# Kernel tuning notes

Measured on AMD Instinct MI355X. Metric: run time of the kernel, lower is better.

## Reference

```python
import jax, jax.numpy as jnp
import numpy as np

HEADS = 8

def setup_inputs() -> dict:
    key = jax.random.key(0)
    k1, k2, k3 = jax.random.split(key, 3)
    B, C, L = 8, 512, 4096
    dim_head = 64
    hidden = HEADS * dim_head  # 512
    x = jax.random.normal(k1, (B, C, L), dtype=jnp.float32)
    # Conv1d(dim, hidden*3, 1, bias=False) -> weight [hidden*3, dim]
    w_qkv = jax.random.normal(k2, (hidden * 3, C), dtype=jnp.float32) * 0.02
    # Conv1d(hidden, dim, 1) -> weight [dim, hidden], bias [dim]
    w_out = jax.random.normal(k3, (C, hidden), dtype=jnp.float32) * 0.02
    b_out = jnp.zeros((C,), dtype=jnp.float32)
    return {"x": x, "w_qkv": w_qkv, "w_out": w_out, "b_out": b_out}

def reference(x, w_qkv, w_out, b_out):
    B, C, L = x.shape
    # 1x1 Conv1d == channel matmul
    qkv = jnp.einsum('oc,bcl->bol', w_qkv, x)            # [B, 3*H*dh, L]
    qkv = qkv.reshape(B, 3, HEADS, -1, L)                # qkv outermost, then heads, then c
    q, k, v = qkv[:, 0], qkv[:, 1], qkv[:, 2]            # each [B, H, dh, L]
    k = jax.nn.softmax(k, axis=-1)                       # softmax over sequence
    context = jnp.einsum('bhdn,bhen->bhde', k, v)        # [B, H, dh, dh]
    out = jnp.einsum('bhde,bhdn->bhen', context, q)      # [B, H, dh, L]
    out = out.reshape(B, -1, L)                          # [B, H*dh, L]
    return jnp.einsum('oc,bcl->bol', w_out, out) + b_out[None, :, None]
```

## Files before the change

### kernel.cpp

```cpp
#include <hip/hip_runtime.h>
#include <hip/hip_bf16.h>


typedef __bf16 bf16x8 __attribute__((ext_vector_type(8)));
typedef __bf16 bf16x4 __attribute__((ext_vector_type(4)));
typedef float  f32x4  __attribute__((ext_vector_type(4)));

#define B_  8
#define L_  4096
#define C_  512

#define GLD_LDS16(g, l)                                             \
    __builtin_amdgcn_global_load_lds(                               \
        (const __attribute__((address_space(1))) void*)(g),         \
        (__attribute__((address_space(3))) void*)(l), 16, 0, 0)

#define FENCE asm volatile("" ::: "memory")
#define BAR   do { FENCE; __builtin_amdgcn_s_barrier(); FENCE; } while (0)
#define DRAIN_LGKM asm volatile("s_waitcnt lgkmcnt(0)" ::: "memory")
#define WAIT_VM(N) asm volatile("s_waitcnt vmcnt(" #N ")" ::: "memory")

__global__ __launch_bounds__(256) void prep_all(const float* __restrict__ x,
                                                __hip_bfloat16* __restrict__ xt,
                                                const float* __restrict__ wqkv_f,
                                                __hip_bfloat16* __restrict__ wkv_b,
                                                __hip_bfloat16* __restrict__ wqT) {
    __shared__ float tile[64 * 132];
    int blk = blockIdx.x;
    int t = threadIdx.x;
    if (blk < 2048) {
        int b = blk >> 8, rem = blk & 255;
        int l0 = (rem & 31) * 128, c0 = (rem >> 5) * 64;
        const float* xp = x + ((size_t)b * C_ + c0) * L_ + l0;
#pragma unroll
        for (int p = 0; p < 8; p++) {
            int i = p * 8 + (t >> 5);
            int j = (t & 31) * 4;
            float4 vv = *(const float4*)(xp + (size_t)i * L_ + j);
            *(float4*)&tile[i * 132 + j] = vv;
        }
        __syncthreads();
        unsigned short* xo = (unsigned short*)xt + ((size_t)b * L_ + l0) * C_ + c0;
#pragma unroll
        for (int qq = 0; qq < 8; qq++) {
            int l = qq * 16 + (t >> 4);
            int cg = (t & 15) * 4;
            bf16x4 ov;
#pragma unroll
            for (int k = 0; k < 4; k++) ov[k] = (__bf16)tile[(cg + k) * 132 + l];
            *(bf16x4*)(xo + (size_t)l * C_ + cg) = ov;
        }
    } else if (blk < 4096) {
        int i = (blk - 2048) * 256 + t;
        wkv_b[i] = __float2bfloat16(wqkv_f[512 * 512 + i]);
    } else {
        int tb = blk - 4096;
        int r0 = (tb >> 4) * 32, c0 = (tb & 15) * 32;
        int tx = t & 31, ty = t >> 5;
        for (int r = 0; r < 32; r += 8)
            tile[(ty + r) * 33 + tx] = wqkv_f[(size_t)(r0 + ty + r) * 512 + c0 + tx];
        __syncthreads();
        for (int r = 0; r < 32; r += 8)
            wqT[(size_t)(c0 + ty + r) * 512 + r0 + tx] = __float2bfloat16(tile[tx * 33 + ty + r]);
    }
}

template <int MODE>
__global__ __launch_bounds__(256, 2) void gemm_p(
    const __hip_bfloat16* __restrict__ A, const __hip_bfloat16* __restrict__ Bt,
    size_t strideA, size_t strideB, int M, int N, int K,
    __hip_bfloat16* __restrict__ kb, __hip_bfloat16* __restrict__ vb,
    float* __restrict__ outb, const float* __restrict__ bias) {
    __shared__ alignas(16) unsigned short sA[2][128 * 64];
    __shared__ alignas(16) unsigned short sB[2][128 * 64];

    int b = blockIdx.z;
    int m0 = blockIdx.y * 128, n0 = blockIdx.x * 128;
    const __hip_bfloat16* Ab = A + strideA * (size_t)b;
    const __hip_bfloat16* Bb = Bt + strideB * (size_t)b;

    int t = threadIdx.x;
    int lane = t & 63, wv = t >> 6;
    int l16 = lane & 15, q4 = lane >> 4;
    int wr = (wv >> 1) * 64, wc = (wv & 1) * 64;

    int srow = lane >> 3;
    int swz  = ((lane & 7) ^ srow) * 8;

    const __hip_bfloat16* gA[4];
    const __hip_bfloat16* gB[4];
    unsigned ldoff[4];
#pragma unroll
    for (int c = 0; c < 4; c++) {
        int r = c * 32 + wv * 8;
        gA[c] = Ab + (size_t)(m0 + r + srow) * K + swz;
        gB[c] = Bb + (size_t)(n0 + r + srow) * K + swz;
        ldoff[c] = (unsigned)r * 64;
    }

    int gsel0 = (q4 ^ (l16 & 7)) * 8;
    int gsel1 = gsel0 ^ 32;
    unsigned rA = (unsigned)(wr + l16) * 64;
    unsigned rB = (unsigned)(wc + l16) * 64;
    int NKT = K >> 6;

    f32x4 acc[4][4] = {};
    bf16x8 aF[4][2], bF[4][2];

#pragma unroll
    for (int c = 0; c < 4; c++) GLD_LDS16(gA[c], &sA[0][ldoff[c]]);
#pragma unroll
    for (int c = 0; c < 4; c++) GLD_LDS16(gB[c], &sB[0][ldoff[c]]);
    if (NKT > 1) {
#pragma unroll
        for (int c = 0; c < 4; c++) GLD_LDS16(gA[c] + 64, &sA[1][ldoff[c]]);
        WAIT_VM(4);
    } else {
        WAIT_VM(0);
    }
    BAR;

#pragma unroll 1
    for (int kt = 0; kt < NKT; ++kt) {
        int cur = kt & 1, nbuf = cur ^ 1;
        const unsigned short* As_b = sA[cur];
        const unsigned short* Bs_b = sB[cur];
        bool st1 = (kt + 1) < NKT;
        bool st2 = (kt + 2) < NKT;

#pragma unroll
        for (int i = 0; i < 4; i++) {
            aF[i][0] = *(const bf16x8*)&As_b[rA + i * 1024 + gsel0];
            aF[i][1] = *(const bf16x8*)&As_b[rA + i * 1024 + gsel1];
        }
#pragma unroll
        for (int j = 0; j < 2; j++) {
            bF[j][0] = *(const bf16x8*)&Bs_b[rB + j * 1024 + gsel0];
            bF[j][1] = *(const bf16x8*)&Bs_b[rB + j * 1024 + gsel1];
        }
        if (st1) {
            int ko = (kt + 1) << 6;
#pragma unroll
            for (int c = 0; c < 4; c++) GLD_LDS16(gB[c] + ko, &sB[nbuf][ldoff[c]]);
        }
        BAR;
        __builtin_amdgcn_s_setprio(1);
#pragma unroll
        for (int ks = 0; ks < 2; ks++)
#pragma unroll
            for (int i = 0; i < 4; i++)
#pragma unroll
                for (int j = 0; j < 2; j++)
                    acc[i][j] = __builtin_amdgcn_mfma_f32_16x16x32_bf16(aF[i][ks], bF[j][ks], acc[i][j], 0, 0, 0);
        __builtin_amdgcn_s_setprio(0);
        DRAIN_LGKM;
        BAR;

#pragma unroll
        for (int j = 2; j < 4; j++) {
            bF[j][0] = *(const bf16x8*)&Bs_b[rB + j * 1024 + gsel0];
            bF[j][1] = *(const bf16x8*)&Bs_b[rB + j * 1024 + gsel1];
        }
        if (st2) {
            int ko = (kt + 2) << 6;
#pragma unroll
            for (int c = 0; c < 4; c++) GLD_LDS16(gA[c] + ko, &sA[cur][ldoff[c]]);
        }
        BAR;
        __builtin_amdgcn_s_setprio(1);
#pragma unroll
        for (int ks = 0; ks < 2; ks++)
#pragma unroll
            for (int i = 0; i < 4; i++)
#pragma unroll
                for (int j = 0; j < 2; j++)
                    acc[i][2 + j] = __builtin_amdgcn_mfma_f32_16x16x32_bf16(aF[i][ks], bF[2 + j][ks], acc[i][2 + j], 0, 0, 0);
        __builtin_amdgcn_s_setprio(0);
        DRAIN_LGKM;
        if (st2) { WAIT_VM(4); } else { WAIT_VM(0); }
        BAR;
    }

#pragma unroll
    for (int i = 0; i < 4; i++)
#pragma unroll
        for (int j = 0; j < 4; j++)
#pragma unroll
            for (int r = 0; r < 4; r++) {
                int row = m0 + wr + i * 16 + q4 * 4 + r;
                int col = n0 + wc + j * 16 + l16;
                float val = acc[i][j][r];
                if (MODE == 1) {
                    __hip_bfloat16* dst = (m0 < 512) ? kb : vb;
                    int od = row & 511;
                    dst[((size_t)b * 512 + od) * (size_t)N + col] = __float2bfloat16(val);
                } else {
                    outb[((size_t)b * M + row) * (size_t)N + col] = val + bias[row];
                }
            }
}

template <int MODE>
__global__ __launch_bounds__(256) void gemm_bt(
    const __hip_bfloat16* __restrict__ A, const __hip_bfloat16* __restrict__ Bt,
    size_t strideA, size_t strideB, int M, int N, int K,
    __hip_bfloat16* __restrict__ obf) {
    __shared__ alignas(16) unsigned short As[128 * 64];
    __shared__ alignas(16) unsigned short Bs[128 * 64];

    int b = blockIdx.z;
    int m0 = blockIdx.y * 128, n0 = blockIdx.x * 128;
    const __hip_bfloat16* Ab = A + strideA * (size_t)b;
    const __hip_bfloat16* Bb = Bt + strideB * (size_t)b;

    int t = threadIdx.x;
    int lane = t & 63, wv = t >> 6;
    int l16 = lane & 15, q4 = lane >> 4;
    int wr = (wv >> 1) * 64, wc = (wv & 1) * 64;

    int srow = lane >> 3;
    int swz  = ((lane & 7) ^ srow) * 8;

    const __hip_bfloat16* gA[4];
    const __hip_bfloat16* gB[4];
    unsigned short* lA[4];
    unsigned short* lB[4];
#pragma unroll
    for (int c = 0; c < 4; c++) {
        int r = wv * 32 + c * 8;
        gA[c] = Ab + (size_t)(m0 + r + srow) * K + swz;
        gB[c] = Bb + (size_t)(n0 + r + srow) * K + swz;
        lA[c] = &As[r * 64];
        lB[c] = &Bs[r * 64];
    }

    int gsel0 = ((q4) ^ (l16 & 7)) * 8;
    int gsel1 = gsel0 ^ 32;
    int rA = (wr + l16) * 64;
    int rB = (wc + l16) * 64;

    f32x4 acc[4][4] = {};

    for (int k0 = 0; k0 < K; k0 += 64) {
        __syncthreads();
#pragma unroll
        for (int c = 0; c < 4; c++) {
            GLD_LDS16(gA[c] + k0, lA[c]);
            GLD_LDS16(gB[c] + k0, lB[c]);
        }
        __syncthreads();

        bf16x8 af[4], bfr[4];
#pragma unroll
        for (int i = 0; i < 4; i++) {
            af[i]  = *(const bf16x8*)&As[rA + i * 1024 + gsel0];
            bfr[i] = *(const bf16x8*)&Bs[rB + i * 1024 + gsel0];
        }
#pragma unroll
        for (int i = 0; i < 4; i++)
#pragma unroll
            for (int j = 0; j < 4; j++)
                acc[i][j] = __builtin_amdgcn_mfma_f32_16x16x32_bf16(af[i], bfr[j], acc[i][j], 0, 0, 0);
#pragma unroll
        for (int i = 0; i < 4; i++) {
            af[i]  = *(const bf16x8*)&As[rA + i * 1024 + gsel1];
            bfr[i] = *(const bf16x8*)&Bs[rB + i * 1024 + gsel1];
        }
#pragma unroll
        for (int i = 0; i < 4; i++)
#pragma unroll
            for (int j = 0; j < 4; j++)
                acc[i][j] = __builtin_amdgcn_mfma_f32_16x16x32_bf16(af[i], bfr[j], acc[i][j], 0, 0, 0);
    }

#pragma unroll
    for (int i = 0; i < 4; i++)
#pragma unroll
        for (int j = 0; j < 4; j++)
#pragma unroll
            for (int r = 0; r < 4; r++) {
                int row = m0 + wr + i * 16 + q4 * 4 + r;
                int col = n0 + wc + j * 16 + l16;
                obf[((size_t)b * 512 + row) * (size_t)N + col] = __float2bfloat16(acc[i][j][r]);
            }
}

__global__ __launch_bounds__(256) void ctx_kernel(const __hip_bfloat16* __restrict__ kraw,
                                                  const __hip_bfloat16* __restrict__ v,
                                                  float* __restrict__ ctxp,
                                                  float* __restrict__ sums) {
    int kc = blockIdx.x, h = blockIdx.y, b = blockIdx.z;
    int t = threadIdx.x, lane = t & 63, wv = t >> 6;
    int l16 = lane & 15, q4 = lane >> 4;
    const __hip_bfloat16* ka = kraw + ((size_t)b * 512 + h * 64) * L_;
    const __hip_bfloat16* va = v + ((size_t)b * 512 + h * 64) * L_;

    f32x4 acc[4][4] = {};
    float ps[4] = {0.f, 0.f, 0.f, 0.f};
    int nbase = kc * 1024 + wv * 256;
#pragma unroll 1
    for (int s = 0; s < 8; s++) {
        int n = nbase + s * 32 + q4 * 8;
        bf16x8 af[4], bfr[4];
#pragma unroll
        for (int i = 0; i < 4; i++) {
            bf16x8 kv = *(const bf16x8*)(ka + (size_t)(i * 16 + l16) * L_ + n);
#pragma unroll
            for (int e = 0; e < 8; e++) {
                float ev = __expf((float)kv[e]);
                af[i][e] = (__bf16)ev;
                ps[i] += ev;
            }
            bfr[i] = *(const bf16x8*)(va + (size_t)(i * 16 + l16) * L_ + n);
        }
#pragma unroll
        for (int i = 0; i < 4; i++)
#pragma unroll
            for (int j = 0; j < 4; j++)
                acc[i][j] = __builtin_amdgcn_mfma_f32_16x16x32_bf16(af[i], bfr[j], acc[i][j], 0, 0, 0);
    }

    __shared__ float sred[4][64];
#pragma unroll
    for (int i = 0; i < 4; i++) {
        ps[i] += __shfl_xor(ps[i], 16, 64);
        ps[i] += __shfl_xor(ps[i], 32, 64);
    }
    if (q4 == 0) {
#pragma unroll
        for (int i = 0; i < 4; i++) sred[wv][i * 16 + l16] = ps[i];
    }
    __syncthreads();
    if (t < 64) {
        float S = sred[0][t] + sred[1][t] + sred[2][t] + sred[3][t];
        sums[(((size_t)kc * 8 + b) * 8 + h) * 64 + t] = S;
    }

    __shared__ float cbuf[4096];
    for (int w = 0; w < 4; w++) {
        if (wv == w) {
#pragma unroll
            for (int i = 0; i < 4; i++)
#pragma unroll
                for (int j = 0; j < 4; j++)
#pragma unroll
                    for (int r = 0; r < 4; r++) {
                        int mm = i * 16 + q4 * 4 + r, nn = j * 16 + l16;
                        float pv = acc[i][j][r];
                        if (w == 0) cbuf[mm * 64 + nn] = pv;
                        else        cbuf[mm * 64 + nn] += pv;
                    }
        }
        __syncthreads();
    }
    float* cg = ctxp + (((size_t)kc * 8 + b) * 8 + h) * 4096;
    for (int i = t; i < 4096; i += 256) cg[i] = cbuf[i];
}

__global__ __launch_bounds__(256) void w2_kernel(const float* __restrict__ wout,
                                                 const float* __restrict__ ctxp,
                                                 const float* __restrict__ sums,
                                                 __hip_bfloat16* __restrict__ w2) {
    int ob = blockIdx.x, h = blockIdx.y, b = blockIdx.z;
    __shared__ float cT[64 * 65];
    __shared__ float wT[64 * 65];
    __shared__ float Sinv[64];
    int t = threadIdx.x;
    const size_t KCS = (size_t)8 * 8 * 4096;
    const float* cg = ctxp + (((size_t)b) * 8 + h) * 4096;
    for (int i = t; i < 4096; i += 256) {
        int d = i >> 6, e = i & 63;
        float s = cg[i] + cg[KCS + i] + cg[2 * KCS + i] + cg[3 * KCS + i];
        cT[e * 65 + d] = s;
        wT[e * 65 + d] = wout[(size_t)(ob * 64 + d) * 512 + h * 64 + e];
    }
    if (t < 64) {
        const size_t SKC = (size_t)8 * 8 * 64;
        const float* sg = sums + ((size_t)b * 8 + h) * 64;
        float S = sg[t] + sg[SKC + t] + sg[2 * SKC + t] + sg[3 * SKC + t];
        Sinv[t] = 1.0f / S;
    }
    __syncthreads();
    int ol = t >> 2;
    int db = (t & 3) * 16;
    for (int dd = 0; dd < 16; dd++) {
        int d = db + dd;
        float s = 0.f;
#pragma unroll
        for (int e = 0; e < 64; e++) s += wT[e * 65 + ol] * cT[e * 65 + d];
        w2[((size_t)b * 512 + ob * 64 + ol) * 512 + h * 64 + d] = __float2bfloat16(s * Sinv[d]);
    }
}

extern "C" void kernel_launch(void* const* d_in, const int* in_sizes, int n_in,
                              void* d_out, int out_size, void* d_ws, size_t ws_size,
                              hipStream_t stream) {
    const float* x     = (const float*)d_in[0];
    const float* w_qkv = (const float*)d_in[1];
    const float* w_out = (const float*)d_in[2];
    const float* b_out = (const float*)d_in[3];
    float* out = (float*)d_out;
    char* ws = (char*)d_ws;

    const size_t QKV = (size_t)B_ * 512 * L_;
    size_t off_xt   = 0;
    size_t off_wkv  = off_xt + (size_t)B_ * L_ * C_ * 2;
    size_t off_wqT  = off_wkv + (size_t)1024 * 512 * 2;
    size_t off_k    = off_wqT + (size_t)512 * 512 * 2;
    size_t off_v    = off_k + QKV * 2;
    size_t off_ctxp = off_v + QKV * 2;
    size_t off_sums = off_ctxp + (size_t)4 * 8 * 8 * 4096 * 4;
    size_t off_w2   = off_k;
    size_t off_w3   = off_k + (size_t)B_ * 512 * 512 * 2;

    __hip_bfloat16* xt   = (__hip_bfloat16*)(ws + off_xt);
    __hip_bfloat16* wkvb = (__hip_bfloat16*)(ws + off_wkv);
    __hip_bfloat16* wqT  = (__hip_bfloat16*)(ws + off_wqT);
    __hip_bfloat16* kb   = (__hip_bfloat16*)(ws + off_k);
    __hip_bfloat16* vb   = (__hip_bfloat16*)(ws + off_v);
    float*          ctxp = (float*)(ws + off_ctxp);
    float*          sums = (float*)(ws + off_sums);
    __hip_bfloat16* w2   = (__hip_bfloat16*)(ws + off_w2);
    __hip_bfloat16* W3   = (__hip_bfloat16*)(ws + off_w3);

    prep_all<<<4352, 256, 0, stream>>>(x, xt, w_qkv, wkvb, wqT);

    gemm_p<1><<<dim3(L_ / 128, 1024 / 128, B_), 256, 0, stream>>>(
        wkvb, xt, 0, (size_t)L_ * C_, 1024, L_, 512, kb, vb, nullptr, nullptr);

    ctx_kernel<<<dim3(4, 8, B_), 256, 0, stream>>>(kb, vb, ctxp, sums);

    w2_kernel<<<dim3(8, 8, B_), 256, 0, stream>>>(w_out, ctxp, sums, w2);

    gemm_bt<3><<<dim3(512 / 128, 512 / 128, B_), 256, 0, stream>>>(
        w2, wqT, (size_t)512 * 512, 0, 512, 512, 512, W3);

    gemm_p<2><<<dim3(L_ / 128, 512 / 128, B_), 256, 0, stream>>>(
        W3, xt, (size_t)512 * 512, (size_t)L_ * C_, 512, L_, 512, nullptr, nullptr, out, b_out);
}
```

Measured before the change: 244.4 us.

## Fuse key exp into QKV GEMM epilogue, split context over more blocks, reuse pipelined GEMM

Moves the exponential of keys into the QKV projection epilogue, so the context kernel only loads exp(k) and sums it. The context kernel now uses 8 sequence chunks instead of 4, doubling its block count, and w2_kernel reduces 8 partials and folds the softmax normalisation into the context before its small matmul, which now writes 4-wide vector stores. The small W3 GEMM switches from the unpipelined gemm_bt to the double-buffered gemm_p, and the transpose tile stride is padded to 133 to avoid LDS bank conflicts. Storing exp(k) in bf16 without max subtraction risks overflow and loses some precision compared with exponentiating in fp32 inside the context kernel.

```diff
diff --git a/kernel.cpp b/kernel.cpp
--- a/kernel.cpp
+++ b/kernel.cpp
@@ -25,7 +25,7 @@
                                                 const float* __restrict__ wqkv_f,
                                                 __hip_bfloat16* __restrict__ wkv_b,
                                                 __hip_bfloat16* __restrict__ wqT) {
-    __shared__ float tile[64 * 132];
+    __shared__ float tile[64 * 133];
     int blk = blockIdx.x;
     int t = threadIdx.x;
     if (blk < 2048) {
@@ -37,7 +37,7 @@
             int i = p * 8 + (t >> 5);
             int j = (t & 31) * 4;
             float4 vv = *(const float4*)(xp + (size_t)i * L_ + j);
-            *(float4*)&tile[i * 132 + j] = vv;
+            *(float4*)&tile[i * 133 + j] = vv;
         }
         __syncthreads();
         unsigned short* xo = (unsigned short*)xt + ((size_t)b * L_ + l0) * C_ + c0;
@@ -47,7 +47,7 @@
             int cg = (t & 15) * 4;
             bf16x4 ov;
 #pragma unroll
-            for (int k = 0; k < 4; k++) ov[k] = (__bf16)tile[(cg + k) * 132 + l];
+            for (int k = 0; k < 4; k++) ov[k] = (__bf16)tile[(cg + k) * 133 + l];
             *(bf16x4*)(xo + (size_t)l * C_ + cg) = ov;
         }
     } else if (blk < 4096) {
@@ -70,6 +70,7 @@
     const __hip_bfloat16* __restrict__ A, const __hip_bfloat16* __restrict__ Bt,
     size_t strideA, size_t strideB, int M, int N, int K,
     __hip_bfloat16* __restrict__ kb, __hip_bfloat16* __restrict__ vb,
+    __hip_bfloat16* __restrict__ obf,
     float* __restrict__ outb, const float* __restrict__ bias) {
     __shared__ alignas(16) unsigned short sA[2][128 * 64];
     __shared__ alignas(16) unsigned short sB[2][128 * 64];
@@ -191,127 +192,41 @@
                 int col = n0 + wc + j * 16 + l16;
                 float val = acc[i][j][r];
                 if (MODE == 1) {
-                    __hip_bfloat16* dst = (m0 < 512) ? kb : vb;
-                    int od = row & 511;
-                    dst[((size_t)b * 512 + od) * (size_t)N + col] = __float2bfloat16(val);
+                    bool isk = (m0 < 512);
+                    __hip_bfloat16* dst = isk ? kb : vb;
+                    if (isk) val = __expf(val);
+                    dst[((size_t)b * 512 + (row & 511)) * (size_t)N + col] = __float2bfloat16(val);
+                } else if (MODE == 3) {
+                    obf[((size_t)b * 512 + row) * (size_t)N + col] = __float2bfloat16(val);
                 } else {
                     outb[((size_t)b * M + row) * (size_t)N + col] = val + bias[row];
                 }
             }
 }
 
-template <int MODE>
-__global__ __launch_bounds__(256) void gemm_bt(
-    const __hip_bfloat16* __restrict__ A, const __hip_bfloat16* __restrict__ Bt,
-    size_t strideA, size_t strideB, int M, int N, int K,
-    __hip_bfloat16* __restrict__ obf) {
-    __shared__ alignas(16) unsigned short As[128 * 64];
-    __shared__ alignas(16) unsigned short Bs[128 * 64];
-
-    int b = blockIdx.z;
-    int m0 = blockIdx.y * 128, n0 = blockIdx.x * 128;
-    const __hip_bfloat16* Ab = A + strideA * (size_t)b;
-    const __hip_bfloat16* Bb = Bt + strideB * (size_t)b;
-
-    int t = threadIdx.x;
-    int lane = t & 63, wv = t >> 6;
-    int l16 = lane & 15, q4 = lane >> 4;
-    int wr = (wv >> 1) * 64, wc = (wv & 1) * 64;
-
-    int srow = lane >> 3;
-    int swz  = ((lane & 7) ^ srow) * 8;
-
-    const __hip_bfloat16* gA[4];
-    const __hip_bfloat16* gB[4];
-    unsigned short* lA[4];
-    unsigned short* lB[4];
-#pragma unroll
-    for (int c = 0; c < 4; c++) {
-        int r = wv * 32 + c * 8;
-        gA[c] = Ab + (size_t)(m0 + r + srow) * K + swz;
-        gB[c] = Bb + (size_t)(n0 + r + srow) * K + swz;
-        lA[c] = &As[r * 64];
-        lB[c] = &Bs[r * 64];
-    }
-
-    int gsel0 = ((q4) ^ (l16 & 7)) * 8;
-    int gsel1 = gsel0 ^ 32;
-    int rA = (wr + l16) * 64;
-    int rB = (wc + l16) * 64;
-
-    f32x4 acc[4][4] = {};
-
-    for (int k0 = 0; k0 < K; k0 += 64) {
-        __syncthreads();
-#pragma unroll
-        for (int c = 0; c < 4; c++) {
-            GLD_LDS16(gA[c] + k0, lA[c]);
-            GLD_LDS16(gB[c] + k0, lB[c]);
-        }
-        __syncthreads();
-
-        bf16x8 af[4], bfr[4];
-#pragma unroll
-        for (int i = 0; i < 4; i++) {
-            af[i]  = *(const bf16x8*)&As[rA + i * 1024 + gsel0];
-            bfr[i] = *(const bf16x8*)&Bs[rB + i * 1024 + gsel0];
-        }
-#pragma unroll
-        for (int i = 0; i < 4; i++)
-#pragma unroll
-            for (int j = 0; j < 4; j++)
-                acc[i][j] = __builtin_amdgcn_mfma_f32_16x16x32_bf16(af[i], bfr[j], acc[i][j], 0, 0, 0);
-#pragma unroll
-        for (int i = 0; i < 4; i++) {
-            af[i]  = *(const bf16x8*)&As[rA + i * 1024 + gsel1];
-            bfr[i] = *(const bf16x8*)&Bs[rB + i * 1024 + gsel1];
-        }
-#pragma unroll
-        for (int i = 0; i < 4; i++)
-#pragma unroll
-            for (int j = 0; j < 4; j++)
-                acc[i][j] = __builtin_amdgcn_mfma_f32_16x16x32_bf16(af[i], bfr[j], acc[i][j], 0, 0, 0);
-    }
-
-#pragma unroll
-    for (int i = 0; i < 4; i++)
-#pragma unroll
-        for (int j = 0; j < 4; j++)
-#pragma unroll
-            for (int r = 0; r < 4; r++) {
-                int row = m0 + wr + i * 16 + q4 * 4 + r;
-                int col = n0 + wc + j * 16 + l16;
-                obf[((size_t)b * 512 + row) * (size_t)N + col] = __float2bfloat16(acc[i][j][r]);
-            }
-}
-
-__global__ __launch_bounds__(256) void ctx_kernel(const __hip_bfloat16* __restrict__ kraw,
+__global__ __launch_bounds__(256) void ctx_kernel(const __hip_bfloat16* __restrict__ ek,
                                                   const __hip_bfloat16* __restrict__ v,
                                                   float* __restrict__ ctxp,
-                                                  float* __restrict__ sums) {
+                                                  float* __restrict__ Sp) {
     int kc = blockIdx.x, h = blockIdx.y, b = blockIdx.z;
     int t = threadIdx.x, lane = t & 63, wv = t >> 6;
     int l16 = lane & 15, q4 = lane >> 4;
-    const __hip_bfloat16* ka = kraw + ((size_t)b * 512 + h * 64) * L_;
+    const __hip_bfloat16* ka = ek + ((size_t)b * 512 + h * 64) * L_;
     const __hip_bfloat16* va = v + ((size_t)b * 512 + h * 64) * L_;
 
     f32x4 acc[4][4] = {};
     float ps[4] = {0.f, 0.f, 0.f, 0.f};
-    int nbase = kc * 1024 + wv * 256;
-#pragma unroll 1
-    for (int s = 0; s < 8; s++) {
+    int nbase = kc * 512 + wv * 128;
+#pragma unroll
+    for (int s = 0; s < 4; s++) {
         int n = nbase + s * 32 + q4 * 8;
         bf16x8 af[4], bfr[4];
 #pragma unroll
         for (int i = 0; i < 4; i++) {
-            bf16x8 kv = *(const bf16x8*)(ka + (size_t)(i * 16 + l16) * L_ + n);
-#pragma unroll
-            for (int e = 0; e < 8; e++) {
-                float ev = __expf((float)kv[e]);
-                af[i][e] = (__bf16)ev;
-                ps[i] += ev;
-            }
+            af[i]  = *(const bf16x8*)(ka + (size_t)(i * 16 + l16) * L_ + n);
             bfr[i] = *(const bf16x8*)(va + (size_t)(i * 16 + l16) * L_ + n);
+#pragma unroll
+            for (int e = 0; e < 8; e++) ps[i] += (float)af[i][e];
         }
 #pragma unroll
         for (int i = 0; i < 4; i++)
@@ -330,13 +245,9 @@
 #pragma unroll
         for (int i = 0; i < 4; i++) sred[wv][i * 16 + l16] = ps[i];
     }
+
+    __shared__ float cbuf[4096];
     __syncthreads();
-    if (t < 64) {
-        float S = sred[0][t] + sred[1][t] + sred[2][t] + sred[3][t];
-        sums[(((size_t)kc * 8 + b) * 8 + h) * 64 + t] = S;
-    }
-
-    __shared__ float cbuf[4096];
     for (int w = 0; w < 4; w++) {
         if (wv == w) {
 #pragma unroll
@@ -353,42 +264,57 @@
         }
         __syncthreads();
     }
-    float* cg = ctxp + (((size_t)kc * 8 + b) * 8 + h) * 4096;
+    float* cg = ctxp + ((size_t)kc * 64 + b * 8 + h) * 4096;
     for (int i = t; i < 4096; i += 256) cg[i] = cbuf[i];
+    if (t < 64)
+        Sp[((size_t)kc * 64 + b * 8 + h) * 64 + t] = sred[0][t] + sred[1][t] + sred[2][t] + sred[3][t];
 }
 
 __global__ __launch_bounds__(256) void w2_kernel(const float* __restrict__ wout,
                                                  const float* __restrict__ ctxp,
-                                                 const float* __restrict__ sums,
+                                                 const float* __restrict__ Sp,
                                                  __hip_bfloat16* __restrict__ w2) {
     int ob = blockIdx.x, h = blockIdx.y, b = blockIdx.z;
     __shared__ float cT[64 * 65];
     __shared__ float wT[64 * 65];
     __shared__ float Sinv[64];
     int t = threadIdx.x;
-    const size_t KCS = (size_t)8 * 8 * 4096;
-    const float* cg = ctxp + (((size_t)b) * 8 + h) * 4096;
+    const size_t SL = (size_t)64 * 4096;
+    const float* cg = ctxp + ((size_t)b * 8 + h) * 4096;
+    if (t < 64) {
+        const float* sg = Sp + ((size_t)b * 8 + h) * 64;
+        float S = 0.f;
+#pragma unroll
+        for (int s = 0; s < 8; s++) S += sg[(size_t)s * 64 * 64 + t];
+        Sinv[t] = 1.0f / S;
+    }
+    __syncthreads();
     for (int i = t; i < 4096; i += 256) {
         int d = i >> 6, e = i & 63;
-        float s = cg[i] + cg[KCS + i] + cg[2 * KCS + i] + cg[3 * KCS + i];
-        cT[e * 65 + d] = s;
+        float s = 0.f;
+#pragma unroll
+        for (int sl = 0; sl < 8; sl++) s += cg[(size_t)sl * SL + i];
+        cT[e * 65 + d] = s * Sinv[d];
         wT[e * 65 + d] = wout[(size_t)(ob * 64 + d) * 512 + h * 64 + e];
-    }
-    if (t < 64) {
-        const size_t SKC = (size_t)8 * 8 * 64;
-        const float* sg = sums + ((size_t)b * 8 + h) * 64;
-        float S = sg[t] + sg[SKC + t] + sg[2 * SKC + t] + sg[3 * SKC + t];
-        Sinv[t] = 1.0f / S;
     }
     __syncthreads();
     int ol = t >> 2;
     int db = (t & 3) * 16;
-    for (int dd = 0; dd < 16; dd++) {
-        int d = db + dd;
-        float s = 0.f;
-#pragma unroll
-        for (int e = 0; e < 64; e++) s += wT[e * 65 + ol] * cT[e * 65 + d];
-        w2[((size_t)b * 512 + ob * 64 + ol) * 512 + h * 64 + d] = __float2bfloat16(s * Sinv[d]);
+    unsigned short* w2p = (unsigned short*)w2 + ((size_t)b * 512 + ob * 64 + ol) * 512 + h * 64;
+    for (int g = 0; g < 4; g++) {
+        int d0 = db + g * 4;
+        float s0 = 0.f, s1 = 0.f, s2 = 0.f, s3 = 0.f;
+#pragma unroll
+        for (int e = 0; e < 64; e++) {
+            float w = wT[e * 65 + ol];
+            s0 += w * cT[e * 65 + d0];
+            s1 += w * cT[e * 65 + d0 + 1];
+            s2 += w * cT[e * 65 + d0 + 2];
+            s3 += w * cT[e * 65 + d0 + 3];
+        }
+        bf16x4 ov;
+        ov[0] = (__bf16)s0; ov[1] = (__bf16)s1; ov[2] = (__bf16)s2; ov[3] = (__bf16)s3;
+        *(bf16x4*)(w2p + d0) = ov;
     }
 }
 
@@ -409,7 +335,7 @@
     size_t off_k    = off_wqT + (size_t)512 * 512 * 2;
     size_t off_v    = off_k + QKV * 2;
     size_t off_ctxp = off_v + QKV * 2;
-    size_t off_sums = off_ctxp + (size_t)4 * 8 * 8 * 4096 * 4;
+    size_t off_Sp   = off_ctxp + (size_t)8 * 64 * 4096 * 4;
     size_t off_w2   = off_k;
     size_t off_w3   = off_k + (size_t)B_ * 512 * 512 * 2;
 
@@ -419,22 +345,22 @@
     __hip_bfloat16* kb   = (__hip_bfloat16*)(ws + off_k);
     __hip_bfloat16* vb   = (__hip_bfloat16*)(ws + off_v);
     float*          ctxp = (float*)(ws + off_ctxp);
-    float*          sums = (float*)(ws + off_sums);
+    float*          Sp   = (float*)(ws + off_Sp);
     __hip_bfloat16* w2   = (__hip_bfloat16*)(ws + off_w2);
     __hip_bfloat16* W3   = (__hip_bfloat16*)(ws + off_w3);
 
     prep_all<<<4352, 256, 0, stream>>>(x, xt, w_qkv, wkvb, wqT);
 
     gemm_p<1><<<dim3(L_ / 128, 1024 / 128, B_), 256, 0, stream>>>(
-        wkvb, xt, 0, (size_t)L_ * C_, 1024, L_, 512, kb, vb, nullptr, nullptr);
-
-    ctx_kernel<<<dim3(4, 8, B_), 256, 0, stream>>>(kb, vb, ctxp, sums);
-
-    w2_kernel<<<dim3(8, 8, B_), 256, 0, stream>>>(w_out, ctxp, sums, w2);
-
-    gemm_bt<3><<<dim3(512 / 128, 512 / 128, B_), 256, 0, stream>>>(
-        w2, wqT, (size_t)512 * 512, 0, 512, 512, 512, W3);
+        wkvb, xt, 0, (size_t)L_ * C_, 1024, L_, 512, kb, vb, nullptr, nullptr, nullptr);
+
+    ctx_kernel<<<dim3(8, 8, B_), 256, 0, stream>>>(kb, vb, ctxp, Sp);
+
+    w2_kernel<<<dim3(8, 8, B_), 256, 0, stream>>>(w_out, ctxp, Sp, w2);
+
+    gemm_p<3><<<dim3(512 / 128, 512 / 128, B_), 256, 0, stream>>>(
+        w2, wqT, (size_t)512 * 512, 0, 512, 512, 512, nullptr, nullptr, W3, nullptr, nullptr);
 
     gemm_p<2><<<dim3(L_ / 128, 512 / 128, B_), 256, 0, stream>>>(
-        W3, xt, (size_t)512 * 512, (size_t)L_ * C_, 512, L_, 512, nullptr, nullptr, out, b_out);
-}
+        W3, xt, (size_t)512 * 512, (size_t)L_ * C_, 512, L_, 512, nullptr, nullptr, nullptr, out, b_out);
+}
```

New measurement: 243.8 us. About the same (-0.2%).
